# Optimization experiments

Hardware: AMD Instinct MI355X
Metric: run time of the kernel (lower is better)

## Reference

```python
import jax, jax.numpy as jnp
import numpy as np

N_EMBED = 1024
HIDDEN = 2752  # find_multiple(int(8/3*1024), 32)
NUM_EXPERTS = 8
TOP_K = 2
AUX_COEFF = 0.01


def _swiglu(x, wg, wu, wd):
    # x: [N,C]; wg,wu: [H,C]; wd: [C,H]  (nn.Linear weight layout, y = x @ W.T)
    return (jax.nn.silu(x @ wg.T) * (x @ wu.T)) @ wd.T


def setup_inputs() -> dict:
    key = jax.random.key(0)
    ks = jax.random.split(key, 8)
    s = 0.02
    return {
        "x": jax.random.normal(ks[0], (2, 2048, N_EMBED), dtype=jnp.float32),
        "gate_w": jax.random.normal(ks[1], (NUM_EXPERTS, N_EMBED), dtype=jnp.float32) * s,
        "expert_gate_w": jax.random.normal(ks[2], (NUM_EXPERTS, HIDDEN, N_EMBED), dtype=jnp.float32) * s,
        "expert_up_w": jax.random.normal(ks[3], (NUM_EXPERTS, HIDDEN, N_EMBED), dtype=jnp.float32) * s,
        "expert_down_w": jax.random.normal(ks[4], (NUM_EXPERTS, N_EMBED, HIDDEN), dtype=jnp.float32) * s,
        "shared_gate_w": jax.random.normal(ks[5], (HIDDEN, N_EMBED), dtype=jnp.float32) * s,
        "shared_up_w": jax.random.normal(ks[6], (HIDDEN, N_EMBED), dtype=jnp.float32) * s,
        "shared_down_w": jax.random.normal(ks[7], (N_EMBED, HIDDEN), dtype=jnp.float32) * s,
    }


def reference(x, gate_w, expert_gate_w, expert_up_w, expert_down_w,
              shared_gate_w, shared_up_w, shared_down_w):
    B, T, C = x.shape
    xf = x.reshape(-1, C)                      # [N, C]
    N = xf.shape[0]

    # shared expert (always-on)
    shared_out = _swiglu(xf, shared_gate_w, shared_up_w, shared_down_w)

    # gating
    logits = xf @ gate_w.T                     # [N, E]
    top_w, top_i = jax.lax.top_k(logits, TOP_K)
    top_w = jax.nn.softmax(top_w.astype(jnp.float32), axis=-1)  # [N, K]

    # load-balancing aux loss
    mask = jax.nn.one_hot(top_i, NUM_EXPERTS, dtype=jnp.float32).sum(axis=1)  # [N, E]
    frac_selected = mask.mean(axis=0)
    mean_probs = jax.nn.softmax(logits.astype(jnp.float32), axis=-1).mean(axis=0)
    aux_loss = AUX_COEFF * (frac_selected * mean_probs).sum()

    # dense per-token per-expert combine weights (0 for unselected experts)
    w_dense = jnp.zeros((N, NUM_EXPERTS), jnp.float32)
    w_dense = w_dense.at[jnp.arange(N)[:, None], top_i].add(top_w)  # [N, E]

    routed = jnp.zeros_like(xf)
    for e in range(NUM_EXPERTS):
        routed = routed + _swiglu(xf, expert_gate_w[e], expert_up_w[e],
                                  expert_down_w[e]) * w_dense[:, e:e + 1]

    final = (shared_out + routed).reshape(B, T, C)
    return final, aux_loss
```

## Files before the change

kernel.cpp:

```cpp
#include <hip/hip_runtime.h>
#include <hip/hip_bf16.h>
#include <math.h>

#define N_TOK 4096
#define CDIM 1024
#define HDIM 2752
#define NEXP 8

typedef __bf16 bf16_t;
typedef __bf16 bf16x8 __attribute__((ext_vector_type(8)));
typedef float f32x4 __attribute__((ext_vector_type(4)));

__device__ __forceinline__ void gload_lds16(const void* g, void* l) {
  __builtin_amdgcn_global_load_lds(
      (const __attribute__((address_space(1))) unsigned int*)g,
      (__attribute__((address_space(3))) unsigned int*)l, 16, 0, 0);
}

struct CastG {
  const float* src[6];
  bf16_t* dst[6];
  int start[7];
  const float* x;
  const float* gw;
  int* top_i; float* top_w; float* probs_tok; bf16_t* xb;
};
__global__ void moe_cast_gate(CastG c) {
  const int b = blockIdx.x;
  if (b < c.start[6]) {
    int k = 0;
#pragma unroll
    for (int i = 0; i < 5; ++i) k += (b >= c.start[i + 1]);
    size_t i4 = (size_t)(b - c.start[k]) * 256 + threadIdx.x;
    float4 v = ((const float4*)c.src[k])[i4];
    union { bf16_t b4[4]; unsigned long long u; } pk;
    pk.b4[0] = (bf16_t)v.x; pk.b4[1] = (bf16_t)v.y;
    pk.b4[2] = (bf16_t)v.z; pk.b4[3] = (bf16_t)v.w;
    ((unsigned long long*)c.dst[k])[i4] = pk.u;
    return;
  }
  const int gb = b - c.start[6];
  const int wid = threadIdx.x >> 6, lane = threadIdx.x & 63;
  const int n = gb * 4 + wid;
  const float* xr = c.x + (size_t)n * CDIM;
  float xv[16];
  for (int j = 0; j < 16; j += 4)
    *(float4*)&xv[j] = *(const float4*)(xr + lane * 16 + j);
  {
    union { bf16_t bb[4]; unsigned long long u; } pk;
    unsigned long long* dst = (unsigned long long*)(c.xb + (size_t)n * CDIM + lane * 16);
    for (int j = 0; j < 16; j += 4) {
      pk.bb[0] = (bf16_t)xv[j]; pk.bb[1] = (bf16_t)xv[j+1];
      pk.bb[2] = (bf16_t)xv[j+2]; pk.bb[3] = (bf16_t)xv[j+3];
      dst[j >> 2] = pk.u;
    }
  }
  double part[NEXP];
  for (int e = 0; e < NEXP; ++e) {
    const float* gr = c.gw + e * CDIM + lane * 16;
    double s = 0.0;
    for (int j = 0; j < 16; j += 4) {
      float4 g = *(const float4*)(gr + j);
      s += (double)xv[j] * g.x + (double)xv[j+1] * g.y + (double)xv[j+2] * g.z + (double)xv[j+3] * g.w;
    }
    part[e] = s;
  }
  for (int off = 32; off; off >>= 1)
    for (int e = 0; e < NEXP; ++e) part[e] += __shfl_xor(part[e], off);
  if (lane == 0) {
    int i0 = 0; double l0 = part[0];
    for (int e = 1; e < NEXP; ++e) if (part[e] > l0) { l0 = part[e]; i0 = e; }
    int i1 = -1; double l1 = -1e300;
    for (int e = 0; e < NEXP; ++e) if (e != i0 && part[e] > l1) { l1 = part[e]; i1 = e; }
    double ed = exp(l1 - l0);
    float w0 = (float)(1.0 / (1.0 + ed));
    float w1 = (float)(ed / (1.0 + ed));
    c.top_i[2*n] = i0; c.top_i[2*n+1] = i1;
    c.top_w[2*n] = w0; c.top_w[2*n+1] = w1;
    double Z = 0.0, pe[NEXP];
    for (int e = 0; e < NEXP; ++e) { pe[e] = exp(part[e] - l0); Z += pe[e]; }
    for (int e = 0; e < NEXP; ++e) c.probs_tok[(size_t)n * NEXP + e] = (float)(pe[e] / Z);
  }
}

__global__ __launch_bounds__(512) void moe_control(
    const float* __restrict__ probs_tok, const int* __restrict__ top_i,
    const float* __restrict__ top_w,
    int* __restrict__ cnts_g, int* __restrict__ offs_g,
    int* __restrict__ rowlist, float* __restrict__ wlist,
    float* __restrict__ out_aux) {
  __shared__ float ps[NEXP];
  __shared__ int cs[NEXP];
  __shared__ int offs_s[NEXP];
  __shared__ int cur[NEXP];
  const int wid = threadIdx.x >> 6, lane = threadIdx.x & 63;

  float s = 0.f; int cc = 0;
  for (int n = lane; n < N_TOK; n += 64) {
    s += probs_tok[(size_t)n * NEXP + wid];
    cc += (top_i[2*n] == wid) + (top_i[2*n+1] == wid);
  }
  for (int o = 32; o; o >>= 1) { s += __shfl_xor(s, o); cc += __shfl_xor(cc, o); }
  if (lane == 0) { ps[wid] = s; cs[wid] = cc; cur[wid] = 0; }
  __syncthreads();
  if (threadIdx.x == 0) {
    int o = 0; double aux = 0.0;
    for (int e = 0; e < NEXP; ++e) {
      offs_s[e] = o; o += cs[e];
      aux += (double)cs[e] * (double)ps[e];
      cnts_g[e] = cs[e]; offs_g[e] = offs_s[e];
    }
    out_aux[0] = (float)(0.01 * aux / ((double)N_TOK * (double)N_TOK));
  }
  __syncthreads();
  const unsigned long long lt = ((unsigned long long)1 << lane) - 1;
  for (int i = 0; i < N_TOK / 512; ++i) {
    int n = i * 512 + wid * 64 + lane;
    int e0 = top_i[2*n], e1 = top_i[2*n + 1];
    float w0 = top_w[2*n], w1 = top_w[2*n + 1];
    for (int e = 0; e < NEXP; ++e) {
      unsigned long long m0 = __ballot(e0 == e);
      unsigned long long m1 = __ballot(e1 == e);
      int tot = __popcll(m0) + __popcll(m1);
      int base = 0;
      if (lane == 0 && tot) base = atomicAdd(&cur[e], tot);
      base = __shfl(base, 0);
      if (e0 == e) {
        int p = offs_s[e] + base + __popcll(m0 & lt);
        rowlist[p] = n; wlist[p] = w0;
      }
      if (e1 == e) {
        int p = offs_s[e] + base + __popcll(m0) + __popcll(m1 & lt);
        rowlist[p] = n; wlist[p] = w1;
      }
    }
  }
}

__launch_bounds__(256)
__global__ void moe_gu(const bf16_t* __restrict__ xb,
                       const bf16_t* __restrict__ Wg_r, const bf16_t* __restrict__ Wu_r,
                       const bf16_t* __restrict__ Wg_s, const bf16_t* __restrict__ Wu_s,
                       bf16_t* __restrict__ hout,
                       const int* __restrict__ rowlist, const int* __restrict__ offs,
                       const int* __restrict__ cnts) {
  const int z = blockIdx.z;
  const bool routed = z < NEXP;
  int cnt, hbase, loff = 0;
  const bf16_t *Wg, *Wu;
  if (routed) {
    cnt = cnts[z]; loff = offs[z]; hbase = loff;
    if ((int)blockIdx.y * 128 >= cnt) return;
    Wg = Wg_r + (size_t)z * HDIM * CDIM;
    Wu = Wu_r + (size_t)z * HDIM * CDIM;
  } else {
    cnt = N_TOK; hbase = 2 * N_TOK;
    Wg = Wg_s; Wu = Wu_s;
  }
  const int m0 = blockIdx.y * 128, n0 = blockIdx.x * 64;

  __shared__ alignas(16) bf16_t lA[128 * 64];
  __shared__ alignas(16) bf16_t lB[128 * 64];

  const int tid = threadIdx.x, wid = tid >> 6, lane = tid & 63;
  const int r8 = lane >> 3, c8 = lane & 7;
  const int fr = lane & 15, hi = lane >> 4;

  const bf16_t* gA[4];
  for (int i = 0; i < 4; ++i) {
    int r = wid * 32 + i * 8 + r8;
    int tok;
    if (routed) { int mm = m0 + r < cnt ? m0 + r : cnt - 1; tok = rowlist[loff + mm]; }
    else tok = m0 + r;
    gA[i] = xb + (size_t)tok * CDIM + c8 * 8;
  }
  const bf16_t* gB[4];
  for (int i = 0; i < 4; ++i) {
    int br = wid * 32 + i * 8 + r8;
    gB[i] = (br < 64 ? Wg + (size_t)(n0 + br) * CDIM
                     : Wu + (size_t)(n0 + br - 64) * CDIM) + c8 * 8;
  }

  f32x4 accG[2][4] = {}; f32x4 accU[2][4] = {};

  for (int kt = 0; kt < CDIM / 64; ++kt) {
    if (kt) __syncthreads();
    for (int i = 0; i < 4; ++i) gload_lds16(gA[i] + kt * 64, lA + (wid * 32 + i * 8) * 64);
    for (int i = 0; i < 4; ++i) gload_lds16(gB[i] + kt * 64, lB + (wid * 32 + i * 8) * 64);
    __syncthreads();
    for (int kk = 0; kk < 2; ++kk) {
      const int kb = kk * 32 + hi * 8;
      bf16x8 a[2], bg[4], bu[4];
      for (int i = 0; i < 2; ++i) a[i] = *(const bf16x8*)(lA + (wid * 32 + i * 16 + fr) * 64 + kb);
      for (int j = 0; j < 4; ++j) {
        bg[j] = *(const bf16x8*)(lB + (j * 16 + fr) * 64 + kb);
        bu[j] = *(const bf16x8*)(lB + (64 + j * 16 + fr) * 64 + kb);
      }
      for (int i = 0; i < 2; ++i)
        for (int j = 0; j < 4; ++j) {
          accG[i][j] = __builtin_amdgcn_mfma_f32_16x16x32_bf16(a[i], bg[j], accG[i][j], 0, 0, 0);
          accU[i][j] = __builtin_amdgcn_mfma_f32_16x16x32_bf16(a[i], bu[j], accU[i][j], 0, 0, 0);
        }
    }
  }
  for (int i = 0; i < 2; ++i)
    for (int j = 0; j < 4; ++j)
      for (int r = 0; r < 4; ++r) {
        int lm = wid * 32 + i * 16 + hi * 4 + r;
        if (routed && m0 + lm >= cnt) continue;
        float g = accG[i][j][r], u = accU[i][j][r];
        float hv = (g / (1.f + __expf(-g))) * u;
        hout[(size_t)(hbase + m0 + lm) * HDIM + n0 + j * 16 + fr] = (bf16_t)hv;
      }
}

__launch_bounds__(256)
__global__ void moe_down(const bf16_t* __restrict__ hin, const bf16_t* __restrict__ Wd_r,
                         const bf16_t* __restrict__ Wd_s,
                         float* __restrict__ outp,
                         const float* __restrict__ wlist, const int* __restrict__ rowlist,
                         const int* __restrict__ offs, const int* __restrict__ cnts) {
  const int z = blockIdx.z;
  const bool routed = z < NEXP;
  int cnt, hbase;
  const bf16_t* Wd;
  if (routed) {
    cnt = cnts[z]; hbase = offs[z];
    if ((int)blockIdx.y * 128 >= cnt) return;
    Wd = Wd_r + (size_t)z * CDIM * HDIM;
  } else {
    cnt = N_TOK; hbase = 2 * N_TOK;
    Wd = Wd_s;
  }
  const int m0 = blockIdx.y * 128, n0 = blockIdx.x * 128;

  __shared__ alignas(16) bf16_t lA[128 * 64];
  __shared__ alignas(16) bf16_t lB[128 * 64];

  const int tid = threadIdx.x, wid = tid >> 6, lane = tid & 63;
  const int wm = wid >> 1, wn = wid & 1;
  const int r8 = lane >> 3, c8 = lane & 7;
  const int fr = lane & 15, hi = lane >> 4;

  const bf16_t* gA[4];
  for (int i = 0; i < 4; ++i) {
    int r = wid * 32 + i * 8 + r8;
    int mm = (routed && m0 + r >= cnt) ? cnt - 1 : m0 + r;
    gA[i] = hin + (size_t)(hbase + mm) * HDIM + c8 * 8;
  }
  const bf16_t* gB[4];
  for (int i = 0; i < 4; ++i) {
    int br = wid * 32 + i * 8 + r8;
    gB[i] = Wd + (size_t)(n0 + br) * HDIM + c8 * 8;
  }

  f32x4 acc[4][4] = {};

  for (int kt = 0; kt < HDIM / 64; ++kt) {
    if (kt) __syncthreads();
    for (int i = 0; i < 4; ++i) gload_lds16(gA[i] + kt * 64, lA + (wid * 32 + i * 8) * 64);
    for (int i = 0; i < 4; ++i) gload_lds16(gB[i] + kt * 64, lB + (wid * 32 + i * 8) * 64);
    __syncthreads();
    for (int kk = 0; kk < 2; ++kk) {
      const int kb = kk * 32 + hi * 8;
      bf16x8 a[4], b[4];
      for (int i = 0; i < 4; ++i) a[i] = *(const bf16x8*)(lA + (wm * 64 + i * 16 + fr) * 64 + kb);
      for (int j = 0; j < 4; ++j) b[j] = *(const bf16x8*)(lB + (wn * 64 + j * 16 + fr) * 64 + kb);
      for (int i = 0; i < 4; ++i)
        for (int j = 0; j < 4; ++j)
          acc[i][j] = __builtin_amdgcn_mfma_f32_16x16x32_bf16(a[i], b[j], acc[i][j], 0, 0, 0);
    }
  }
  for (int i = 0; i < 4; ++i)
    for (int j = 0; j < 4; ++j)
      for (int r = 0; r < 4; ++r) {
        int lm = wm * 64 + i * 16 + hi * 4 + r;
        if (routed && m0 + lm >= cnt) continue;
        float v = acc[i][j][r];
        int col = n0 + wn * 64 + j * 16 + fr;
        if (routed) {
          int pos = hbase + m0 + lm;
          int tok = rowlist[pos];
          atomicAdd(&outp[(size_t)tok * CDIM + col], v * wlist[pos]);
        } else {
          atomicAdd(&outp[(size_t)(m0 + lm) * CDIM + col], v);
        }
      }
}

extern "C" void kernel_launch(void* const* d_in, const int* in_sizes, int n_in,
                              void* d_out, int out_size, void* d_ws, size_t ws_size,
                              hipStream_t stream) {
  const float* x   = (const float*)d_in[0];
  const float* gw  = (const float*)d_in[1];
  const float* egw = (const float*)d_in[2];
  const float* euw = (const float*)d_in[3];
  const float* edw = (const float*)d_in[4];
  const float* sgw = (const float*)d_in[5];
  const float* suw = (const float*)d_in[6];
  const float* sdw = (const float*)d_in[7];
  float* out = (float*)d_out;

  char* ws = (char*)d_ws;
  size_t off = 0;
  auto alloc = [&](size_t bytes) -> void* {
    void* p = ws + off; off = (off + bytes + 255) & ~(size_t)255; return p;
  };
  const size_t EW = (size_t)NEXP * HDIM * CDIM;
  const size_t SW = (size_t)HDIM * CDIM;
  bf16_t* xb    = (bf16_t*)alloc((size_t)N_TOK * CDIM * 2);
  bf16_t* egw_b = (bf16_t*)alloc(EW * 2);
  bf16_t* euw_b = (bf16_t*)alloc(EW * 2);
  bf16_t* edw_b = (bf16_t*)alloc(EW * 2);
  bf16_t* sgw_b = (bf16_t*)alloc(SW * 2);
  bf16_t* suw_b = (bf16_t*)alloc(SW * 2);
  bf16_t* sdw_b = (bf16_t*)alloc(SW * 2);
  bf16_t* h     = (bf16_t*)alloc((size_t)(3 * N_TOK + 256) * HDIM * 2);
  int*    ctrl  = (int*)alloc(256);
  int* cnts = ctrl; int* offs = ctrl + 8;
  int*   top_i    = (int*)alloc((size_t)N_TOK * 2 * 4);
  float* top_w    = (float*)alloc((size_t)N_TOK * 2 * 4);
  int*   rowlist  = (int*)alloc((size_t)2 * N_TOK * 4);
  float* wlist    = (float*)alloc((size_t)2 * N_TOK * 4);
  float* probs_tok = (float*)alloc((size_t)N_TOK * NEXP * 4);

  hipMemsetAsync(out, 0, (size_t)N_TOK * CDIM * 4, stream);

  CastG cg;
  cg.src[0] = egw; cg.dst[0] = egw_b;
  cg.src[1] = euw; cg.dst[1] = euw_b;
  cg.src[2] = edw; cg.dst[2] = edw_b;
  cg.src[3] = sgw; cg.dst[3] = sgw_b;
  cg.src[4] = suw; cg.dst[4] = suw_b;
  cg.src[5] = sdw; cg.dst[5] = sdw_b;
  int ew_blk = (int)(EW / 1024), sw_blk = (int)(SW / 1024);
  cg.start[0] = 0;
  cg.start[1] = ew_blk;     cg.start[2] = 2 * ew_blk; cg.start[3] = 3 * ew_blk;
  cg.start[4] = 3 * ew_blk + sw_blk;
  cg.start[5] = 3 * ew_blk + 2 * sw_blk;
  cg.start[6] = 3 * ew_blk + 3 * sw_blk;
  cg.x = x; cg.gw = gw;
  cg.top_i = top_i; cg.top_w = top_w; cg.probs_tok = probs_tok; cg.xb = xb;
  moe_cast_gate<<<cg.start[6] + N_TOK / 4, 256, 0, stream>>>(cg);

  moe_control<<<1, 512, 0, stream>>>(probs_tok, top_i, top_w, cnts, offs,
                                     rowlist, wlist, out + (size_t)N_TOK * CDIM);

  moe_gu<<<dim3(HDIM / 64, N_TOK / 128, NEXP + 1), 256, 0, stream>>>(
      xb, egw_b, euw_b, sgw_b, suw_b, h, rowlist, offs, cnts);
  moe_down<<<dim3(CDIM / 128, N_TOK / 128, NEXP + 1), 256, 0, stream>>>(
      h, edw_b, sdw_b, out, wlist, rowlist, offs, cnts);
}
```

Before: 519.8 us.

## Split single-block MoE routing control into parallel reduce and scatter kernels

```diff
diff --git a/kernel.cpp b/kernel.cpp
--- a/kernel.cpp
+++ b/kernel.cpp
@@ -83,56 +83,89 @@
   }
 }
 
-__global__ __launch_bounds__(512) void moe_control(
+__global__ __launch_bounds__(256) void moe_reduce16(
     const float* __restrict__ probs_tok, const int* __restrict__ top_i,
-    const float* __restrict__ top_w,
+    int* __restrict__ pcnt, float* __restrict__ psum) {
+  const int b = blockIdx.x, t = threadIdx.x;
+  const int wid = t >> 6, lane = t & 63;
+  const int n = b * 256 + t;
+  const int e0 = top_i[2*n], e1 = top_i[2*n + 1];
+  float4 p0 = ((const float4*)(probs_tok + (size_t)n * NEXP))[0];
+  float4 p1 = ((const float4*)(probs_tok + (size_t)n * NEXP))[1];
+  float pv[8] = {p0.x, p0.y, p0.z, p0.w, p1.x, p1.y, p1.z, p1.w};
+  __shared__ int lc[4][NEXP];
+  __shared__ float ls[4][NEXP];
+  for (int e = 0; e < NEXP; ++e) {
+    int c = (e0 == e) + (e1 == e);
+    float s = pv[e];
+    for (int o = 32; o; o >>= 1) { c += __shfl_xor(c, o); s += __shfl_xor(s, o); }
+    if (lane == 0) { lc[wid][e] = c; ls[wid][e] = s; }
+  }
+  __syncthreads();
+  if (t < NEXP) {
+    pcnt[b * NEXP + t] = lc[0][t] + lc[1][t] + lc[2][t] + lc[3][t];
+    psum[b * NEXP + t] = ls[0][t] + ls[1][t] + ls[2][t] + ls[3][t];
+  }
+}
+
+__global__ __launch_bounds__(256) void moe_scatter16(
+    const int* __restrict__ top_i, const float* __restrict__ top_w,
+    const int* __restrict__ pcnt, const float* __restrict__ psum,
     int* __restrict__ cnts_g, int* __restrict__ offs_g,
     int* __restrict__ rowlist, float* __restrict__ wlist,
     float* __restrict__ out_aux) {
-  __shared__ float ps[NEXP];
-  __shared__ int cs[NEXP];
-  __shared__ int offs_s[NEXP];
-  __shared__ int cur[NEXP];
-  const int wid = threadIdx.x >> 6, lane = threadIdx.x & 63;
-
-  float s = 0.f; int cc = 0;
-  for (int n = lane; n < N_TOK; n += 64) {
-    s += probs_tok[(size_t)n * NEXP + wid];
-    cc += (top_i[2*n] == wid) + (top_i[2*n+1] == wid);
-  }
-  for (int o = 32; o; o >>= 1) { s += __shfl_xor(s, o); cc += __shfl_xor(cc, o); }
-  if (lane == 0) { ps[wid] = s; cs[wid] = cc; cur[wid] = 0; }
+  const int b = blockIdx.x, t = threadIdx.x;
+  const int wid = t >> 6, lane = t & 63;
+  __shared__ int tot_s[NEXP], pre_s[NEXP], offs_s[NEXP];
+  __shared__ int wc[4][NEXP];
+  if (t < NEXP) {
+    int e = t, tot = 0, pre = 0;
+    for (int bb = 0; bb < 16; ++bb) {
+      int v = pcnt[bb * NEXP + e];
+      pre += (bb < b) ? v : 0;
+      tot += v;
+    }
+    tot_s[e] = tot; pre_s[e] = pre;
+  }
   __syncthreads();
-  if (threadIdx.x == 0) {
-    int o = 0; double aux = 0.0;
-    for (int e = 0; e < NEXP; ++e) {
-      offs_s[e] = o; o += cs[e];
-      aux += (double)cs[e] * (double)ps[e];
-      cnts_g[e] = cs[e]; offs_g[e] = offs_s[e];
-    }
-    out_aux[0] = (float)(0.01 * aux / ((double)N_TOK * (double)N_TOK));
+  if (t == 0) {
+    int o = 0;
+    for (int e = 0; e < NEXP; ++e) { offs_s[e] = o; o += tot_s[e]; }
+    if (b == 0) {
+      double aux = 0.0;
+      for (int e = 0; e < NEXP; ++e) {
+        float ps = 0.f;
+        for (int bb = 0; bb < 16; ++bb) ps += psum[bb * NEXP + e];
+        aux += (double)tot_s[e] * (double)ps;
+        cnts_g[e] = tot_s[e]; offs_g[e] = offs_s[e];
+      }
+      out_aux[0] = (float)(0.01 * aux / ((double)N_TOK * (double)N_TOK));
+    }
+  }
+  __syncthreads();
+  const int n = b * 256 + t;
+  const int e0 = top_i[2*n], e1 = top_i[2*n + 1];
+  const float w0 = top_w[2*n], w1 = top_w[2*n + 1];
+  for (int e = 0; e < NEXP; ++e) {
+    unsigned long long m0 = __ballot(e0 == e);
+    unsigned long long m1 = __ballot(e1 == e);
+    if (lane == 0) wc[wid][e] = __popcll(m0) + __popcll(m1);
   }
   __syncthreads();
   const unsigned long long lt = ((unsigned long long)1 << lane) - 1;
-  for (int i = 0; i < N_TOK / 512; ++i) {
-    int n = i * 512 + wid * 64 + lane;
-    int e0 = top_i[2*n], e1 = top_i[2*n + 1];
-    float w0 = top_w[2*n], w1 = top_w[2*n + 1];
-    for (int e = 0; e < NEXP; ++e) {
-      unsigned long long m0 = __ballot(e0 == e);
-      unsigned long long m1 = __ballot(e1 == e);
-      int tot = __popcll(m0) + __popcll(m1);
-      int base = 0;
-      if (lane == 0 && tot) base = atomicAdd(&cur[e], tot);
-      base = __shfl(base, 0);
-      if (e0 == e) {
-        int p = offs_s[e] + base + __popcll(m0 & lt);
-        rowlist[p] = n; wlist[p] = w0;
-      }
-      if (e1 == e) {
-        int p = offs_s[e] + base + __popcll(m0) + __popcll(m1 & lt);
-        rowlist[p] = n; wlist[p] = w1;
-      }
+  for (int e = 0; e < NEXP; ++e) {
+    unsigned long long m0 = __ballot(e0 == e);
+    unsigned long long m1 = __ballot(e1 == e);
+    int wp = 0;
+    for (int w = 0; w < wid; ++w) wp += wc[w][e];
+    int base = offs_s[e] + pre_s[e] + wp;
+    if (e0 == e) {
+      int p = base + __popcll(m0 & lt);
+      rowlist[p] = n; wlist[p] = w0;
+    }
+    if (e1 == e) {
+      int p = base + __popcll(m0) + __popcll(m1 & lt);
+      rowlist[p] = n; wlist[p] = w1;
     }
   }
 }
@@ -323,6 +356,8 @@
   int*   rowlist  = (int*)alloc((size_t)2 * N_TOK * 4);
   float* wlist    = (float*)alloc((size_t)2 * N_TOK * 4);
   float* probs_tok = (float*)alloc((size_t)N_TOK * NEXP * 4);
+  int*   pcnt     = (int*)alloc(16 * NEXP * 4);
+  float* psum     = (float*)alloc(16 * NEXP * 4);
 
   hipMemsetAsync(out, 0, (size_t)N_TOK * CDIM * 4, stream);
 
@@ -343,8 +378,9 @@
   cg.top_i = top_i; cg.top_w = top_w; cg.probs_tok = probs_tok; cg.xb = xb;
   moe_cast_gate<<<cg.start[6] + N_TOK / 4, 256, 0, stream>>>(cg);
 
-  moe_control<<<1, 512, 0, stream>>>(probs_tok, top_i, top_w, cnts, offs,
-                                     rowlist, wlist, out + (size_t)N_TOK * CDIM);
+  moe_reduce16<<<16, 256, 0, stream>>>(probs_tok, top_i, pcnt, psum);
+  moe_scatter16<<<16, 256, 0, stream>>>(top_i, top_w, pcnt, psum, cnts, offs,
+                                        rowlist, wlist, out + (size_t)N_TOK * CDIM);
 
   moe_gu<<<dim3(HDIM / 64, N_TOK / 128, NEXP + 1), 256, 0, stream>>>(
       xb, egw_b, euw_b, sgw_b, suw_b, h, rowlist, offs, cnts);
```

Result: faster. 487.0 us (-6.3%).
